# Kernel tuning notes

Measured on AMD Instinct MI355X. Metric: run time of the kernel, lower is better.

The kernel has to match this reference:

```python
import jax, jax.numpy as jnp
import numpy as np

B, H, S, D = 2, 16, 2048, 64
MASK_NEG = 1e9


def setup_inputs() -> dict:
    key = jax.random.key(0)
    kq, kk, kv, km = jax.random.split(key, 4)
    Q = jax.random.normal(kq, (B, H, S, D), dtype=jnp.float32)
    K = jax.random.normal(kk, (B, H, S, D), dtype=jnp.float32)
    V = jax.random.normal(kv, (B, H, S, D), dtype=jnp.float32)
    # float 0/1 mask, broadcast over heads; 1 = masked-out position
    attn_mask = jax.random.randint(km, (B, 1, S, S), 0, 2).astype(jnp.float32)
    return {"Q": Q, "K": K, "V": V, "attn_mask": attn_mask}


def reference(Q, K, V, attn_mask):
    # scores: [B, H, S, S]
    attn_score = jnp.einsum('bhqd,bhkd->bhqk', Q, K)
    scale = jnp.sqrt(jnp.asarray(K.shape[-1], dtype=jnp.float32))
    attn_scale = attn_score / scale - MASK_NEG * attn_mask
    attn_prob = jax.nn.softmax(attn_scale, axis=-1)
    attn_out = jnp.einsum('bhqk,bhkd->bhqd', attn_prob, V)
    return attn_out
```

## Files before the change

### kernel.cpp

```cpp
#include <hip/hip_runtime.h>


#define S_LEN 2048
#define D_DIM 64
#define WPR   32
#define NIT   32

typedef __attribute__((ext_vector_type(8)))  short bf16x8;
typedef __attribute__((ext_vector_type(4)))  float f32x4;
typedef __attribute__((ext_vector_type(16))) float f32x16;
typedef unsigned long long ull;

__device__ __forceinline__ f32x16 mfma32(bf16x8 a, bf16x8 b, f32x16 c) {
  return __builtin_amdgcn_mfma_f32_32x32x16_bf16(a, b, c, 0, 0, 0);
}
__device__ __forceinline__ f32x4 mfma16(bf16x8 a, bf16x8 b, f32x4 c) {
  return __builtin_amdgcn_mfma_f32_16x16x32_bf16(a, b, c, 0, 0, 0);
}
__device__ __forceinline__ unsigned short f2bf(float f) {
  unsigned u = __builtin_bit_cast(unsigned, f);
  unsigned r = u + 0x7FFFu + ((u >> 16) & 1u);
  return (unsigned short)(r >> 16);
}
__device__ __forceinline__ float bf2f(unsigned short s) {
  unsigned u = ((unsigned)s) << 16;
  return __builtin_bit_cast(float, u);
}
__device__ __forceinline__ unsigned packbf(float a, float b) {
#if __has_builtin(__builtin_amdgcn_cvt_pk_bf16_f32)
  typedef __bf16 bfv2 __attribute__((ext_vector_type(2)));
  bfv2 v = __builtin_amdgcn_cvt_pk_bf16_f32(a, b);
  return __builtin_bit_cast(unsigned, v);
#else
  unsigned ua = __builtin_bit_cast(unsigned, a);
  unsigned ub = __builtin_bit_cast(unsigned, b);
  ua = ua + 0x7FFFu + ((ua >> 16) & 1u);
  ub = ub + 0x7FFFu + ((ub >> 16) & 1u);
  return (ua >> 16) | (ub & 0xFFFF0000u);
#endif
}
__device__ __forceinline__ float fexp2(float x) {
#if __has_builtin(__builtin_amdgcn_exp2f)
  return __builtin_amdgcn_exp2f(x);
#else
  return exp2f(x);
#endif
}
__device__ __forceinline__ bool detect_bf16(const void* maskp) {
  const unsigned short* s = (const unsigned short*)maskp;
  unsigned short v = s[2 * (threadIdx.x & 63)];
  return __ballot(v == (unsigned short)0x3F80) != 0ull;
}
__device__ __forceinline__ int4 cvt_f8(const float* p) {
  float4 f0 = *(const float4*)p;
  float4 f1 = *(const float4*)(p + 4);
  int4 r;
  r.x = (int)packbf(f0.x, f0.y);
  r.y = (int)packbf(f0.z, f0.w);
  r.z = (int)packbf(f1.x, f1.y);
  r.w = (int)packbf(f1.z, f1.w);
  return r;
}

#define C1 0.18033688011112042f
#define C2 1.4426950408889634e9f

__global__ __launch_bounds__(256) void prep_all(
    const void* __restrict__ M, const void* __restrict__ Kin,
    const void* __restrict__ Vin, ull* __restrict__ bits,
    unsigned short* __restrict__ Kf, unsigned short* __restrict__ Vf) {
  __shared__ __align__(16) unsigned short T[64 * 72];
  const bool isb = detect_bf16(M);
  const unsigned bx = blockIdx.x;
  const int tid = threadIdx.x;

  if (bx < 32768u) {
    unsigned idx = bx * 256u + tid;
    bool on = isb ? (bf2f(((const unsigned short*)M)[idx]) > 0.5f)
                  : (((const float*)M)[idx] > 0.5f);
    ull bm = __ballot(on);
    if ((tid & 63) == 0) {
      unsigned c = idx & 2047u, r = (idx >> 11) & 2047u, bb = idx >> 22;
      bits[(((size_t)(bb * WPR + (c >> 6))) << 11) + r] = bm;
    }
  } else if (bx < 32768u + 2048u) {
    unsigned g = (bx - 32768u) * 256u + tid;
    unsigned lane = g & 63u, f = (g >> 6) & 7u, it = (g >> 9) & 31u, bh = g >> 14;
    unsigned t = f >> 2, dc = f & 3, hi = lane >> 5, l31 = lane & 31;
    size_t src = (size_t)bh * (S_LEN * D_DIM) +
                 (size_t)(it * 64 + t * 32 + l31) * D_DIM + dc * 16 + hi * 8;
    int4 out;
    if (isb) out = *(const int4*)((const unsigned short*)Kin + src);
    else     out = cvt_f8((const float*)Kin + src);
    *(int4*)&Kf[(size_t)g * 8] = out;
  } else {
    unsigned idx = bx - (32768u + 2048u);
    unsigned bh = idx >> 5, it = idx & 31u;
    {
      int k = tid >> 2, d0 = (tid & 3) * 16;
      size_t src = (size_t)bh * (S_LEN * D_DIM) + (size_t)(it * 64 + k) * D_DIM + d0;
      int4 a, c;
      if (isb) {
        const unsigned short* s = (const unsigned short*)Vin + src;
        a = *(const int4*)s; c = *(const int4*)(s + 8);
      } else {
        const float* s = (const float*)Vin + src;
        a = cvt_f8(s); c = cvt_f8(s + 8);
      }
      *(int4*)&T[k * 72 + d0] = a;
      *(int4*)&T[k * 72 + d0 + 8] = c;
    }
    __syncthreads();
    #pragma unroll
    for (int h = 0; h < 2; ++h) {
      int c = tid + h * 256;
      int lane = c & 63, f = c >> 6;
      int t = f >> 2, kc = (f >> 1) & 1, dt = f & 1;
      int hi = lane >> 5, l31 = lane & 31;
      unsigned short v[8];
      #pragma unroll
      for (int j = 0; j < 8; ++j)
        v[j] = T[(t * 32 + kc * 16 + hi * 8 + j) * 72 + dt * 32 + l31];
      *(int4*)&Vf[(((size_t)(bh * 32 + it)) * 8 + f) * 512 + lane * 8] = *(int4*)v;
    }
  }
}

__global__ __launch_bounds__(256, 4) void attn_fast(
    const void* __restrict__ Qp, const unsigned short* __restrict__ Kf,
    const unsigned short* __restrict__ Vf, const ull* __restrict__ bits,
    const void* __restrict__ maskp, void* __restrict__ Op) {
  __shared__ float Comb[2][32][64];
  __shared__ float Lc[4][32];

  const bool isb = detect_bf16(maskp);
  const int tid  = threadIdx.x;
  const int wave = tid >> 6;
  const int lane = tid & 63;
  const int hi   = lane >> 5;
  const int l31  = lane & 31;
  const int q0   = blockIdx.x * 32;
  const int bh   = blockIdx.y;
  const int b    = bh >> 4;
  const size_t base = (size_t)bh * S_LEN * D_DIM;
  const int xidx = ((lane ^ 32) & 63) * 4;

  bf16x8 qf[4];
  #pragma unroll
  for (int dc = 0; dc < 4; ++dc) {
    size_t off = base + (size_t)(q0 + l31) * D_DIM + dc * 16 + hi * 8;
    float v[8];
    if (isb) {
      unsigned short u[8];
      *(int4*)u = *(const int4*)((const unsigned short*)Qp + off);
      #pragma unroll
      for (int j = 0; j < 8; ++j) v[j] = bf2f(u[j]) * C1;
    } else {
      const float* f = (const float*)Qp + off;
      float4 f0 = *(const float4*)f;
      float4 f1 = *(const float4*)(f + 4);
      v[0] = f0.x * C1; v[1] = f0.y * C1; v[2] = f0.z * C1; v[3] = f0.w * C1;
      v[4] = f1.x * C1; v[5] = f1.y * C1; v[6] = f1.z * C1; v[7] = f1.w * C1;
    }
    uint4 d;
    d.x = packbf(v[0], v[1]); d.y = packbf(v[2], v[3]);
    d.z = packbf(v[4], v[5]); d.w = packbf(v[6], v[7]);
    qf[dc] = __builtin_bit_cast(bf16x8, d);
  }

  f32x16 acc_o[2];
  f32x16 acc_l;
  #pragma unroll
  for (int r = 0; r < 16; ++r) { acc_o[0][r] = 0.f; acc_o[1][r] = 0.f; acc_l[r] = 0.f; }

  bf16x8 onesB;
  {
    short ov = (l31 == 0) ? (short)0x3F80 : (short)0;
    #pragma unroll
    for (int i = 0; i < 8; ++i) onesB[i] = ov;
  }

  for (int i = 0; i < NIT / 4; ++i) {
    const int it = wave * (NIT / 4) + i;
    const size_t fb = ((size_t)(bh * 32 + it)) * 8 * 512;

    ull w = bits[(((size_t)(b * WPR + it)) << 11) + q0 + l31] >> (hi * 4);
    unsigned wt[2] = {(unsigned)w, (unsigned)(w >> 32)};

    #pragma unroll
    for (int t = 0; t < 2; ++t) {
      const unsigned short* Kb = Kf + fb + (size_t)(t * 4) * 512 + lane * 8;
      f32x16 sc;
      #pragma unroll
      for (int r = 0; r < 16; ++r) sc[r] = 0.f;
      #pragma unroll
      for (int dc = 0; dc < 4; ++dc) {
        bf16x8 kfr = *(const bf16x8*)(Kb + dc * 512);
        sc = mfma32(kfr, qf[dc], sc);
      }

      float p[16];
      #pragma unroll
      for (int r = 0; r < 16; ++r) {
        float e = fexp2(sc[r]);
        unsigned bit = (wt[t] >> ((r & 3) + 8 * (r >> 2))) & 1u;
        p[r] = bit ? 0.0f : e;
      }

      #pragma unroll
      for (int kc = 0; kc < 2; ++kc) {
        unsigned pk0 = packbf(p[8 * kc + 0], p[8 * kc + 1]);
        unsigned pk1 = packbf(p[8 * kc + 2], p[8 * kc + 3]);
        unsigned pk2 = packbf(p[8 * kc + 4], p[8 * kc + 5]);
        unsigned pk3 = packbf(p[8 * kc + 6], p[8 * kc + 7]);
        unsigned x0 = (unsigned)__builtin_amdgcn_ds_bpermute(xidx, (int)pk0);
        unsigned x1 = (unsigned)__builtin_amdgcn_ds_bpermute(xidx, (int)pk1);
        unsigned x2 = (unsigned)__builtin_amdgcn_ds_bpermute(xidx, (int)pk2);
        unsigned x3 = (unsigned)__builtin_amdgcn_ds_bpermute(xidx, (int)pk3);
        uint4 d;
        d.x = hi ? x2 : pk0;
        d.y = hi ? x3 : pk1;
        d.z = hi ? pk2 : x0;
        d.w = hi ? pk3 : x1;
        bf16x8 pf = __builtin_bit_cast(bf16x8, d);

        const unsigned short* Vb = Vf + fb + (size_t)(t * 4 + kc * 2) * 512 + lane * 8;
        #pragma unroll
        for (int dt = 0; dt < 2; ++dt) {
          bf16x8 vfr = *(const bf16x8*)(Vb + dt * 512);
          acc_o[dt] = mfma32(pf, vfr, acc_o[dt]);
        }
        acc_l = mfma32(pf, onesB, acc_l);
      }
    }
  }

  __syncthreads();
  if (wave >= 2) {
    #pragma unroll
    for (int dt = 0; dt < 2; ++dt)
      #pragma unroll
      for (int r = 0; r < 16; ++r)
        Comb[wave - 2][dt * 16 + r][lane] = acc_o[dt][r];
  }
  if (l31 == 0) {
    #pragma unroll
    for (int r = 0; r < 16; ++r)
      Lc[wave][(r & 3) + 8 * (r >> 2) + 4 * hi] = acc_l[r];
  }
  __syncthreads();
  if (wave < 2) {
    #pragma unroll
    for (int dt = 0; dt < 2; ++dt)
      #pragma unroll
      for (int r = 0; r < 16; ++r)
        acc_o[dt][r] += Comb[wave][dt * 16 + r][lane];
  }
  __syncthreads();
  if (wave == 1) {
    #pragma unroll
    for (int dt = 0; dt < 2; ++dt)
      #pragma unroll
      for (int r = 0; r < 16; ++r)
        Comb[0][dt * 16 + r][lane] = acc_o[dt][r];
  }
  __syncthreads();
  if (wave == 0) {
    #pragma unroll
    for (int r = 0; r < 16; ++r) {
      int m = (r & 3) + 8 * (r >> 2) + 4 * hi;
      float o0 = acc_o[0][r] + Comb[0][r][lane];
      float o1 = acc_o[1][r] + Comb[0][16 + r][lane];
      float lv = Lc[0][m] + Lc[1][m] + Lc[2][m] + Lc[3][m];
      float inv = 1.0f / lv;
      size_t idx = base + (size_t)(q0 + m) * D_DIM + l31;
      if (isb) {
        ((unsigned short*)Op)[idx]      = f2bf(o0 * inv);
        ((unsigned short*)Op)[idx + 32] = f2bf(o1 * inv);
      } else {
        ((float*)Op)[idx]      = o0 * inv;
        ((float*)Op)[idx + 32] = o1 * inv;
      }
    }
  }
}

__global__ __launch_bounds__(256, 2) void attn_fallback(
    const void* __restrict__ Qp, const void* __restrict__ Kp,
    const void* __restrict__ Vp, const void* __restrict__ maskp,
    void* __restrict__ Op) {
  __shared__ __align__(16) short QKlds[128 * 72];
  __shared__ __align__(16) short Vtlds[64 * 72];
  __shared__ __align__(16) short Plds2[128 * 72];

  const bool isb = detect_bf16(maskp);
  const int tid  = threadIdx.x;
  const int wave = tid >> 6;
  const int lane = tid & 63;
  const int l15  = lane & 15;
  const int quad = lane >> 4;
  const int q0   = blockIdx.x * 128;
  const int bh   = blockIdx.y;
  const int b    = bh >> 4;
  const size_t base = (size_t)bh * S_LEN * D_DIM;

  const short* Qs = (const short*)Qp; const float* Qf = (const float*)Qp;
  const short* Ks = (const short*)Kp; const float* Kf2 = (const float*)Kp;
  const short* Vs = (const short*)Vp; const float* Vf2 = (const float*)Vp;

  if (isb) {
    const short* Qg = Qs + base + (size_t)q0 * D_DIM;
    #pragma unroll
    for (int p = 0; p < 4; ++p) {
      int e = p * 2048 + tid * 8;
      *(int4*)&QKlds[(e >> 6) * 72 + (e & 63)] = *(const int4*)(Qg + e);
    }
  } else {
    const float* Qg = Qf + base + (size_t)q0 * D_DIM;
    #pragma unroll
    for (int p = 0; p < 4; ++p) {
      int e = p * 2048 + tid * 8;
      *(int4*)&QKlds[(e >> 6) * 72 + (e & 63)] = cvt_f8(Qg + e);
    }
  }
  __syncthreads();
  bf16x8 qf[2][2];
  #pragma unroll
  for (int mi = 0; mi < 2; ++mi)
    #pragma unroll
    for (int kt = 0; kt < 2; ++kt)
      qf[mi][kt] = *(const bf16x8*)&QKlds[(wave * 32 + mi * 16 + l15) * 72 + kt * 32 + quad * 8];
  __syncthreads();

  f32x4 acc_o[2][4];
  f32x4 acc_l[2];
  const f32x4 zero4 = {0.f, 0.f, 0.f, 0.f};
  #pragma unroll
  for (int mi = 0; mi < 2; ++mi) {
    acc_l[mi] = zero4;
    #pragma unroll
    for (int nt = 0; nt < 4; ++nt) acc_o[mi][nt] = zero4;
  }
  bf16x8 onesB;
  {
    short ov = (l15 == 0) ? (short)0x3F80 : (short)0;
    #pragma unroll
    for (int i = 0; i < 8; ++i) onesB[i] = ov;
  }

  for (int it = 0; it < NIT; ++it) {
    const int k0 = it * 64;
    if (isb) {
      const short* Kg = Ks + base + (size_t)k0 * D_DIM;
      #pragma unroll
      for (int p = 0; p < 2; ++p) {
        int e = p * 2048 + tid * 8;
        *(int4*)&QKlds[(e >> 6) * 72 + (e & 63)] = *(const int4*)(Kg + e);
      }
    } else {
      const float* Kg = Kf2 + base + (size_t)k0 * D_DIM;
      #pragma unroll
      for (int p = 0; p < 2; ++p) {
        int e = p * 2048 + tid * 8;
        *(int4*)&QKlds[(e >> 6) * 72 + (e & 63)] = cvt_f8(Kg + e);
      }
    }
    {
      const int r0 = (tid >> 3) * 2;
      const int d0 = (tid & 7) * 8;
      unsigned short as_[8], bs_[8];
      if (isb) {
        const short* Vg = Vs + base + (size_t)k0 * D_DIM;
        *(int4*)as_ = *(const int4*)(Vg + r0 * D_DIM + d0);
        *(int4*)bs_ = *(const int4*)(Vg + (r0 + 1) * D_DIM + d0);
      } else {
        const float* Vg = Vf2 + base + (size_t)k0 * D_DIM;
        *(int4*)as_ = cvt_f8(Vg + r0 * D_DIM + d0);
        *(int4*)bs_ = cvt_f8(Vg + (r0 + 1) * D_DIM + d0);
      }
      #pragma unroll
      for (int j = 0; j < 8; ++j) {
        int d = d0 + j;
        int blk = (r0 >> 3) ^ (d >> 3);
        unsigned pk = (unsigned)as_[j] | ((unsigned)bs_[j] << 16);
        *(unsigned*)&Vtlds[d * 72 + blk * 8 + (r0 & 7)] = pk;
      }
    }
    __syncthreads();

    f32x4 sc[2][4];
    #pragma unroll
    for (int mi = 0; mi < 2; ++mi)
      #pragma unroll
      for (int nt = 0; nt < 4; ++nt) sc[mi][nt] = zero4;
    #pragma unroll
    for (int nt = 0; nt < 4; ++nt) {
      bf16x8 kf0 = *(const bf16x8*)&QKlds[(nt * 16 + l15) * 72 + quad * 8];
      bf16x8 kf1 = *(const bf16x8*)&QKlds[(nt * 16 + l15) * 72 + 32 + quad * 8];
      #pragma unroll
      for (int mi = 0; mi < 2; ++mi) {
        sc[mi][nt] = mfma16(qf[mi][0], kf0, sc[mi][nt]);
        sc[mi][nt] = mfma16(qf[mi][1], kf1, sc[mi][nt]);
      }
    }

    #pragma unroll
    for (int mi = 0; mi < 2; ++mi) {
      #pragma unroll
      for (int nt = 0; nt < 4; ++nt) {
        #pragma unroll
        for (int reg = 0; reg < 4; ++reg) {
          int rg = q0 + wave * 32 + mi * 16 + quad * 4 + reg;
          size_t mix = (size_t)b * S_LEN * S_LEN + (size_t)rg * S_LEN + k0 + nt * 16 + l15;
          float mv = isb ? bf2f(((const unsigned short*)maskp)[mix])
                         : ((const float*)maskp)[mix];
          float y = sc[mi][nt][reg] * C1 - mv * C2;
          Plds2[(wave * 32 + mi * 16 + quad * 4 + reg) * 72 + nt * 16 + l15] =
              (short)f2bf(fexp2(y));
        }
      }
    }
    __syncthreads();

    #pragma unroll
    for (int kt = 0; kt < 2; ++kt) {
      bf16x8 pf[2];
      #pragma unroll
      for (int mi = 0; mi < 2; ++mi)
        pf[mi] = *(const bf16x8*)&Plds2[(wave * 32 + mi * 16 + l15) * 72 + kt * 32 + quad * 8];
      #pragma unroll
      for (int nt = 0; nt < 4; ++nt) {
        int d = nt * 16 + l15;
        int kb = (kt * 4 + quad) ^ (d >> 3);
        bf16x8 vf = *(const bf16x8*)&Vtlds[d * 72 + kb * 8];
        #pragma unroll
        for (int mi = 0; mi < 2; ++mi)
          acc_o[mi][nt] = mfma16(pf[mi], vf, acc_o[mi][nt]);
      }
      #pragma unroll
      for (int mi = 0; mi < 2; ++mi)
        acc_l[mi] = mfma16(pf[mi], onesB, acc_l[mi]);
    }
    __syncthreads();
  }

  #pragma unroll
  for (int mi = 0; mi < 2; ++mi) {
    #pragma unroll
    for (int reg = 0; reg < 4; ++reg) {
      float lv = __shfl(acc_l[mi][reg], lane & 48, 64);
      float inv = 1.0f / lv;
      #pragma unroll
      for (int nt = 0; nt < 4; ++nt) {
        float o = acc_o[mi][nt][reg] * inv;
        size_t idx = base + (size_t)(q0 + wave * 32 + mi * 16 + quad * 4 + reg) * D_DIM + nt * 16 + l15;
        if (isb) ((unsigned short*)Op)[idx] = f2bf(o);
        else     ((float*)Op)[idx] = o;
      }
    }
  }
}

extern "C" void kernel_launch(void* const* d_in, const int* in_sizes, int n_in,
                              void* d_out, int out_size, void* d_ws, size_t ws_size,
                              hipStream_t stream) {
  const void* Q = d_in[0];
  const void* K = d_in[1];
  const void* V = d_in[2];
  const void* M = d_in[3];

  dim3 block(256);
  const size_t bits_bytes = (size_t)2 * S_LEN * S_LEN / 8;
  const size_t tens_bytes = (size_t)2 * 16 * S_LEN * D_DIM * 2;

  if (ws_size >= bits_bytes + 2 * tens_bytes) {
    char* ws = (char*)d_ws;
    ull* bits = (ull*)ws;
    unsigned short* Kf = (unsigned short*)(ws + bits_bytes);
    unsigned short* Vf = (unsigned short*)(ws + bits_bytes + tens_bytes);
    prep_all<<<dim3(32768 + 2048 + 1024), block, 0, stream>>>(M, K, V, bits, Kf, Vf);
    attn_fast<<<dim3(S_LEN / 32, 32), block, 0, stream>>>(Q, Kf, Vf, bits, M, d_out);
  } else {
    attn_fallback<<<dim3(S_LEN / 128, 32), block, 0, stream>>>(Q, K, V, M, d_out);
  }
}
```

Before: 192.4 us.

## Precast Q in prep kernel, replace ones-MFMA row sum, remap block order

The prep kernel now also converts and pre-scales Q to bf16 into a workspace buffer, so the attention kernel loads ready-made Q fragments instead of converting them itself. The row-sum MFMA against a ones vector is replaced by a scalar per-lane accumulation of p plus one cross-half bpermute, which removes one MFMA per P chunk. The grid is flattened to 1D with a remapping that interleaves heads across consecutive blocks, which should improve L2/cache locality for K/V and the mask bits. The cost is an extra workspace buffer and more prep work, and the row sum now adds unrounded fp32 p values instead of the bf16-rounded ones.

Result: faster. 187.1 us (-2.8%).

```diff
diff --git a/kernel.cpp b/kernel.cpp
--- a/kernel.cpp
+++ b/kernel.cpp
@@ -67,8 +67,9 @@
 
 __global__ __launch_bounds__(256) void prep_all(
     const void* __restrict__ M, const void* __restrict__ Kin,
-    const void* __restrict__ Vin, ull* __restrict__ bits,
-    unsigned short* __restrict__ Kf, unsigned short* __restrict__ Vf) {
+    const void* __restrict__ Vin, const void* __restrict__ Qin,
+    ull* __restrict__ bits, unsigned short* __restrict__ Kf,
+    unsigned short* __restrict__ Vf, unsigned short* __restrict__ Qc) {
   __shared__ __align__(16) unsigned short T[64 * 72];
   const bool isb = detect_bf16(M);
   const unsigned bx = blockIdx.x;
@@ -93,7 +94,7 @@
     if (isb) out = *(const int4*)((const unsigned short*)Kin + src);
     else     out = cvt_f8((const float*)Kin + src);
     *(int4*)&Kf[(size_t)g * 8] = out;
-  } else {
+  } else if (bx < 32768u + 2048u + 1024u) {
     unsigned idx = bx - (32768u + 2048u);
     unsigned bh = idx >> 5, it = idx & 31u;
     {
@@ -123,11 +124,25 @@
         v[j] = T[(t * 32 + kc * 16 + hi * 8 + j) * 72 + dt * 32 + l31];
       *(int4*)&Vf[(((size_t)(bh * 32 + it)) * 8 + f) * 512 + lane * 8] = *(int4*)v;
     }
+  } else {
+    size_t i0 = ((size_t)(bx - (32768u + 2048u + 1024u)) * 256 + tid) * 8;
+    unsigned short v[8];
+    if (isb) {
+      *(int4*)v = *(const int4*)((const unsigned short*)Qin + i0);
+      #pragma unroll
+      for (int j = 0; j < 8; ++j) v[j] = f2bf(bf2f(v[j]) * C1);
+    } else {
+      const float* f = (const float*)Qin + i0;
+      #pragma unroll
+      for (int j = 0; j < 4; ++j)
+        *((unsigned*)v + j) = packbf(f[2 * j] * C1, f[2 * j + 1] * C1);
+    }
+    *(int4*)&Qc[i0] = *(int4*)v;
   }
 }
 
 __global__ __launch_bounds__(256, 4) void attn_fast(
-    const void* __restrict__ Qp, const unsigned short* __restrict__ Kf,
+    const unsigned short* __restrict__ Qc, const unsigned short* __restrict__ Kf,
     const unsigned short* __restrict__ Vf, const ull* __restrict__ bits,
     const void* __restrict__ maskp, void* __restrict__ Op) {
   __shared__ float Comb[2][32][64];
@@ -139,46 +154,23 @@
   const int lane = tid & 63;
   const int hi   = lane >> 5;
   const int l31  = lane & 31;
-  const int q0   = blockIdx.x * 32;
-  const int bh   = blockIdx.y;
+  const int id   = blockIdx.x;
+  const int slot = id >> 3;
+  const int bh   = (id & 7) * 4 + (slot & 3);
+  const int q0   = (slot >> 2) * 32;
   const int b    = bh >> 4;
   const size_t base = (size_t)bh * S_LEN * D_DIM;
   const int xidx = ((lane ^ 32) & 63) * 4;
 
   bf16x8 qf[4];
   #pragma unroll
-  for (int dc = 0; dc < 4; ++dc) {
-    size_t off = base + (size_t)(q0 + l31) * D_DIM + dc * 16 + hi * 8;
-    float v[8];
-    if (isb) {
-      unsigned short u[8];
-      *(int4*)u = *(const int4*)((const unsigned short*)Qp + off);
-      #pragma unroll
-      for (int j = 0; j < 8; ++j) v[j] = bf2f(u[j]) * C1;
-    } else {
-      const float* f = (const float*)Qp + off;
-      float4 f0 = *(const float4*)f;
-      float4 f1 = *(const float4*)(f + 4);
-      v[0] = f0.x * C1; v[1] = f0.y * C1; v[2] = f0.z * C1; v[3] = f0.w * C1;
-      v[4] = f1.x * C1; v[5] = f1.y * C1; v[6] = f1.z * C1; v[7] = f1.w * C1;
-    }
-    uint4 d;
-    d.x = packbf(v[0], v[1]); d.y = packbf(v[2], v[3]);
-    d.z = packbf(v[4], v[5]); d.w = packbf(v[6], v[7]);
-    qf[dc] = __builtin_bit_cast(bf16x8, d);
-  }
+  for (int dc = 0; dc < 4; ++dc)
+    qf[dc] = *(const bf16x8*)&Qc[base + (size_t)(q0 + l31) * D_DIM + dc * 16 + hi * 8];
 
   f32x16 acc_o[2];
-  f32x16 acc_l;
+  float lsum = 0.f;
   #pragma unroll
-  for (int r = 0; r < 16; ++r) { acc_o[0][r] = 0.f; acc_o[1][r] = 0.f; acc_l[r] = 0.f; }
-
-  bf16x8 onesB;
-  {
-    short ov = (l31 == 0) ? (short)0x3F80 : (short)0;
-    #pragma unroll
-    for (int i = 0; i < 8; ++i) onesB[i] = ov;
-  }
+  for (int r = 0; r < 16; ++r) { acc_o[0][r] = 0.f; acc_o[1][r] = 0.f; }
 
   for (int i = 0; i < NIT / 4; ++i) {
     const int it = wave * (NIT / 4) + i;
@@ -205,6 +197,7 @@
         float e = fexp2(sc[r]);
         unsigned bit = (wt[t] >> ((r & 3) + 8 * (r >> 2))) & 1u;
         p[r] = bit ? 0.0f : e;
+        lsum += p[r];
       }
 
       #pragma unroll
@@ -230,9 +223,14 @@
           bf16x8 vfr = *(const bf16x8*)(Vb + dt * 512);
           acc_o[dt] = mfma32(pf, vfr, acc_o[dt]);
         }
-        acc_l = mfma32(pf, onesB, acc_l);
-      }
-    }
+      }
+    }
+  }
+
+  {
+    int li = __builtin_bit_cast(int, lsum);
+    float other = __builtin_bit_cast(float, __builtin_amdgcn_ds_bpermute(xidx, li));
+    lsum += other;
   }
 
   __syncthreads();
@@ -243,11 +241,7 @@
       for (int r = 0; r < 16; ++r)
         Comb[wave - 2][dt * 16 + r][lane] = acc_o[dt][r];
   }
-  if (l31 == 0) {
-    #pragma unroll
-    for (int r = 0; r < 16; ++r)
-      Lc[wave][(r & 3) + 8 * (r >> 2) + 4 * hi] = acc_l[r];
-  }
+  if (hi == 0) Lc[wave][l31] = lsum;
   __syncthreads();
   if (wave < 2) {
     #pragma unroll
@@ -473,13 +467,15 @@
   const size_t bits_bytes = (size_t)2 * S_LEN * S_LEN / 8;
   const size_t tens_bytes = (size_t)2 * 16 * S_LEN * D_DIM * 2;
 
-  if (ws_size >= bits_bytes + 2 * tens_bytes) {
+  if (ws_size >= bits_bytes + 3 * tens_bytes) {
     char* ws = (char*)d_ws;
     ull* bits = (ull*)ws;
     unsigned short* Kf = (unsigned short*)(ws + bits_bytes);
     unsigned short* Vf = (unsigned short*)(ws + bits_bytes + tens_bytes);
-    prep_all<<<dim3(32768 + 2048 + 1024), block, 0, stream>>>(M, K, V, bits, Kf, Vf);
-    attn_fast<<<dim3(S_LEN / 32, 32), block, 0, stream>>>(Q, Kf, Vf, bits, M, d_out);
+    unsigned short* Qc = (unsigned short*)(ws + bits_bytes + 2 * tens_bytes);
+    prep_all<<<dim3(32768 + 2048 + 1024 + 2048), block, 0, stream>>>(
+        M, K, V, Q, bits, Kf, Vf, Qc);
+    attn_fast<<<dim3(2048), block, 0, stream>>>(Qc, Kf, Vf, bits, M, d_out);
   } else {
     attn_fallback<<<dim3(S_LEN / 128, 32), block, 0, stream>>>(Q, K, V, M, d_out);
   }
```
